# Kernel tuning notes

Measured on AMD Instinct MI355X. Metric: run time of the kernel, lower is better.

Reference implementation:

```python
import jax, jax.numpy as jnp
import numpy as np

B, N, C = 8, 4096, 512

def setup_inputs() -> dict:
    key = jax.random.key(0)
    ks = jax.random.split(key, 6)
    s = 1.0 / np.sqrt(C)
    return {
        "x": jax.random.normal(ks[0], (B, N, C), jnp.float32),
        "Wq": jax.random.normal(ks[1], (C, C), jnp.float32) * s,
        "Wk": jax.random.normal(ks[2], (C, C), jnp.float32) * s,
        "Wv": jax.random.normal(ks[3], (C, C), jnp.float32) * s,
        "W1": jax.random.normal(ks[4], (C, C), jnp.float32) * s,
        "W2": jax.random.normal(ks[5], (C, C), jnp.float32) * s,
    }

def reference(x, Wq, Wk, Wv, W1, W2):
    # torch nn.Linear: y = x @ W.T (bias=False)
    q = x @ Wq.T                      # [B,N,C]
    k = x @ Wk.T
    v = x @ Wv.T
    dim = q.shape[-1]
    q = jax.nn.softmax(q, axis=-1) * (dim ** -0.5)   # softmax over channels
    k = jax.nn.softmax(k, axis=-2)                   # softmax over sequence
    context = jnp.einsum('bnd,bne->bde', k, v)       # [B,C,C]
    attn = jnp.einsum('bnd,bde->bne', q, context)    # [B,N,C]
    x = attn + x
    return (x @ W1.T) @ W2.T + x
```

## Files before the change

kernel.cpp:

```cpp
#include <hip/hip_runtime.h>

typedef unsigned int uint;
typedef __bf16 bf16_t;
typedef bf16_t bf16x8 __attribute__((ext_vector_type(8)));
typedef float floatx4 __attribute__((ext_vector_type(4)));

struct __align__(8) us4 { unsigned short x, y, z, w; };

__device__ __forceinline__ unsigned short f2b(float f) {
    unsigned u = __float_as_uint(f);
    u = u + 0x7FFFu + ((u >> 16) & 1u);
    return (unsigned short)(u >> 16);
}
__device__ __forceinline__ float b2f(unsigned short h) {
    return __uint_as_float(((unsigned)h) << 16);
}

__device__ __forceinline__ void g2l16(const void* g, void* l) {
    __builtin_amdgcn_global_load_lds((__attribute__((address_space(1))) void*)g,
                                     (__attribute__((address_space(3))) void*)l,
                                     16, 0, 0);
}

template <int MODE, int NTN, bool BMS>
__global__ __launch_bounds__(512, 2) void gemm256(
    const unsigned short* __restrict__ A, const unsigned short* __restrict__ B,
    void* __restrict__ O, const unsigned short* __restrict__ R,
    unsigned short* __restrict__ O2, unsigned short* __restrict__ O3,
    float* __restrict__ Sq, float* __restrict__ Sk,
    const float* __restrict__ Sn,
    int K, long long sB, float scale)
{
    __shared__ __attribute__((aligned(16))) unsigned short Ls[4][16384];

    const uint id = blockIdx.x;
    const uint xcd = id & 7;
    const uint g = id >> 3;
    const uint nt = g % NTN;
    const uint mg = g / NTN;
    const uint ms = mg * 8 + xcd;

    int bb, arow0;
    if constexpr (BMS) { bb = (int)(ms & 7); arow0 = bb * 4096 + (int)(ms >> 3) * 256; }
    else               { bb = 0;             arow0 = (int)ms * 256; }
    const int n0 = (int)nt * 256;

    const unsigned short* Bb = B + (long long)bb * sB;
    const int tid = threadIdx.x;
    const int l = tid & 63;
    const int w = tid >> 6;

    const int r0 = tid >> 3;
    const int lc = (tid & 7) ^ (r0 & 7);
    const unsigned short* gsrc = (lc < 4)
        ? A  + (long long)(arow0 + r0) * 512 + lc * 8
        : Bb + (long long)(n0   + r0) * 512 + (lc - 4) * 8;

#define STAGE(bufi, tt) {                                                   \
        const unsigned short* s_ = gsrc + (tt) * 32;                        \
        unsigned short* d_ = &Ls[bufi][0] + tid * 8;                        \
        g2l16(s_,              d_);                                         \
        g2l16(s_ + 64  * 512,  d_ + 4096);                                  \
        g2l16(s_ + 128 * 512,  d_ + 8192);                                  \
        g2l16(s_ + 192 * 512,  d_ + 12288);                                 \
    }

    const int fr = l & 15;
    const int kq = (l >> 4) * 8;
    const int axA = (kq * 2) ^ ((fr & 7) << 4);
    const int axB = axA ^ 64;
    const int wr = w >> 2;
    const int wc = w & 3;

    floatx4 acc[8][4] = {};
    const int NTk = K >> 5;

    STAGE(0, 0); STAGE(1, 1); STAGE(2, 2);
    asm volatile("s_waitcnt vmcnt(8)" ::: "memory");
    __builtin_amdgcn_s_barrier();

    for (int t = 0; t < NTk; ++t) {
        if (t + 3 < NTk) STAGE((t + 3) & 3, t + 3);

        const char* Lb = (const char*)&Ls[t & 3][0];
        const char* pa = Lb + (wr * 128 + fr) * 128 + axA;
        const char* pb = Lb + (wc * 64  + fr) * 128 + axB;

        bf16x8 af[8], bv[4];
#pragma unroll
        for (int i = 0; i < 8; ++i) af[i] = *(const bf16x8*)(pa + i * 2048);
#pragma unroll
        for (int j = 0; j < 4; ++j) bv[j] = *(const bf16x8*)(pb + j * 2048);

        __builtin_amdgcn_s_setprio(1);
#pragma unroll
        for (int i = 0; i < 8; ++i)
#pragma unroll
            for (int j = 0; j < 4; ++j)
                acc[i][j] = __builtin_amdgcn_mfma_f32_16x16x32_bf16(
                    af[i], bv[j], acc[i][j], 0, 0, 0);
        __builtin_amdgcn_s_setprio(0);

        if (t < NTk - 1) {
            if (t + 3 < NTk)      asm volatile("s_waitcnt vmcnt(8)" ::: "memory");
            else if (t + 2 < NTk) asm volatile("s_waitcnt vmcnt(4)" ::: "memory");
            else                  asm volatile("s_waitcnt vmcnt(0)" ::: "memory");
            __builtin_amdgcn_s_barrier();
        }
    }
#undef STAGE

    const int col = l & 15;
    const int rbase = (l >> 4) * 4;
    const int gm0 = arow0 + wr * 128 + rbase;
    const int gn0 = n0 + wc * 64 + col;

    if constexpr (MODE == 4) {
        if (n0 < 512) {
            unsigned short* Oq = (unsigned short*)O;
            float rs[8][4];
#pragma unroll
            for (int i = 0; i < 8; ++i)
#pragma unroll
                for (int r = 0; r < 4; ++r) rs[i][r] = 0.f;
#pragma unroll
            for (int i = 0; i < 8; ++i) {
                int gm = gm0 + i * 16;
#pragma unroll
                for (int j = 0; j < 4; ++j) {
                    int gn = gn0 + j * 16;
#pragma unroll
                    for (int r = 0; r < 4; ++r) {
                        float e = __expf(acc[i][j][r]);
                        rs[i][r] += e;
                        Oq[(long long)(gm + r) * 512 + gn] = f2b(e);
                    }
                }
            }
#pragma unroll
            for (int i = 0; i < 8; ++i)
#pragma unroll
                for (int r = 0; r < 4; ++r) {
                    float v = rs[i][r];
                    v += __shfl_xor(v, 1);
                    v += __shfl_xor(v, 2);
                    v += __shfl_xor(v, 4);
                    v += __shfl_xor(v, 8);
                    if ((l & 15) == 0)
                        atomicAdd(&Sq[gm0 + i * 16 + r], v);
                }
        } else if (n0 < 1024) {
            const int b = arow0 >> 12;
            const int mq0 = (arow0 & 4095) + wr * 128 + rbase;
            float cs[4] = {0.f, 0.f, 0.f, 0.f};
#pragma unroll
            for (int i = 0; i < 8; ++i) {
                int mq = mq0 + i * 16;
#pragma unroll
                for (int j = 0; j < 4; ++j) {
                    int d = gn0 + j * 16 - 512;
                    float e0 = __expf(acc[i][j][0]);
                    float e1 = __expf(acc[i][j][1]);
                    float e2 = __expf(acc[i][j][2]);
                    float e3 = __expf(acc[i][j][3]);
                    cs[j] += e0 + e1 + e2 + e3;
                    us4 pk = { f2b(e0), f2b(e1), f2b(e2), f2b(e3) };
                    *(us4*)(O2 + ((long long)b * 512 + d) * 4096 + mq) = pk;
                }
            }
#pragma unroll
            for (int j = 0; j < 4; ++j) {
                float v = cs[j];
                v += __shfl_xor(v, 16);
                v += __shfl_xor(v, 32);
                if (l < 16)
                    atomicAdd(&Sk[b * 512 + gn0 + j * 16 - 512], v);
            }
        } else {
            const int b = arow0 >> 12;
            const int mq0 = (arow0 & 4095) + wr * 128 + rbase;
#pragma unroll
            for (int i = 0; i < 8; ++i) {
                int mq = mq0 + i * 16;
#pragma unroll
                for (int j = 0; j < 4; ++j) {
                    int e_ = gn0 + j * 16 - 1024;
                    us4 pk = { f2b(acc[i][j][0]), f2b(acc[i][j][1]),
                               f2b(acc[i][j][2]), f2b(acc[i][j][3]) };
                    *(us4*)(O3 + ((long long)b * 512 + e_) * 4096 + mq) = pk;
                }
            }
        }
    } else if constexpr (MODE == 5) {
#pragma unroll
        for (int i = 0; i < 8; ++i) {
            int gm = gm0 + i * 16;
            float invs[4];
#pragma unroll
            for (int r = 0; r < 4; ++r) invs[r] = scale / Sn[gm + r];
#pragma unroll
            for (int j = 0; j < 4; ++j) {
                int gn = gn0 + j * 16;
#pragma unroll
                for (int r = 0; r < 4; ++r) {
                    long long idx = (long long)(gm + r) * 512 + gn;
                    ((unsigned short*)O)[idx] =
                        f2b(acc[i][j][r] * invs[r] + b2f(R[idx]));
                }
            }
        }
    } else {
#pragma unroll
        for (int i = 0; i < 8; ++i) {
            int gm = gm0 + i * 16;
#pragma unroll
            for (int j = 0; j < 4; ++j) {
                int gn = gn0 + j * 16;
#pragma unroll
                for (int r = 0; r < 4; ++r) {
                    long long idx = (long long)(gm + r) * 512 + gn;
                    float v = acc[i][j][r];
                    if constexpr (MODE == 0) {
                        ((unsigned short*)O)[idx] = f2b(v);
                    } else {
                        ((float*)O)[idx] = v + b2f(R[idx]);
                    }
                }
            }
        }
    }
}

__global__ __launch_bounds__(256, 4) void ctx_gemm_sk(
    const unsigned short* __restrict__ V, const unsigned short* __restrict__ Kt,
    float* __restrict__ P)
{
    __shared__ __attribute__((aligned(16))) unsigned short As[128 * 64];
    __shared__ __attribute__((aligned(16))) unsigned short Bs[128 * 64];

    const uint id = blockIdx.x;
    const uint xcd = id & 7;
    const uint g = id >> 3;
    const uint sub = g & 15;
    const int z = (int)(g >> 4) * 8 + (int)xcd;
    const int b = z >> 2;
    const int s = z & 3;
    const int m0 = (int)(sub >> 2) * 128;
    const int n0 = (int)(sub & 3) * 128;

    const unsigned short* Ab = V  + (long long)b * 512 * 4096 + s * 1024;
    const unsigned short* Bb = Kt + (long long)b * 512 * 4096 + s * 1024;

    const int tid = threadIdx.x;
    const int l = tid & 63;
    const int w = tid >> 6;
    const int wm = (w >> 1) * 64;
    const int wn = (w & 1) * 64;

    const int srow = tid >> 3;
    const int scol = (tid & 7) * 8;
    const unsigned short* ga = Ab + (long long)(m0 + srow) * 4096 + scol;
    const unsigned short* gb = Bb + (long long)(n0 + srow) * 4096 + scol;
    unsigned short* la = As + tid * 8;
    unsigned short* lb = Bs + tid * 8;

    const int fr = l & 15;
    const int kq = (l >> 4) * 8;

    floatx4 acc[4][4] = {};

    for (int kt = 0; kt < 1024; kt += 64) {
        __syncthreads();
#pragma unroll
        for (int c = 0; c < 4; ++c) {
            g2l16(ga + (long long)(c * 32) * 4096, la + c * 2048);
            g2l16(gb + (long long)(c * 32) * 4096, lb + c * 2048);
        }
        ga += 64; gb += 64;
        __syncthreads();

#pragma unroll
        for (int h = 0; h < 2; ++h) {
            bf16x8 af[4], bfr[4];
#pragma unroll
            for (int i = 0; i < 4; ++i) {
                af[i]  = *(const bf16x8*)(As + (wm + i * 16 + fr) * 64 + kq + 32 * h);
                bfr[i] = *(const bf16x8*)(Bs + (wn + i * 16 + fr) * 64 + kq + 32 * h);
            }
#pragma unroll
            for (int i = 0; i < 4; ++i)
#pragma unroll
                for (int j = 0; j < 4; ++j)
                    acc[i][j] = __builtin_amdgcn_mfma_f32_16x16x32_bf16(
                        af[i], bfr[j], acc[i][j], 0, 0, 0);
        }
    }

    const int col = l & 15;
    const int rbase = (l >> 4) * 4;
    float* Pb = P + ((long long)z * 16 + (sub >> 2) * 4 + (sub & 3)) * 16384;
#pragma unroll
    for (int i = 0; i < 4; ++i)
#pragma unroll
        for (int j = 0; j < 4; ++j)
#pragma unroll
            for (int r = 0; r < 4; ++r)
                Pb[(wm + i * 16 + rbase + r) * 128 + wn + j * 16 + col] =
                    acc[i][j][r];
}

__global__ __launch_bounds__(256) void ctx_reduce(const float* __restrict__ P,
                                                  const float* __restrict__ Sk,
                                                  unsigned short* __restrict__ Ct)
{
    long long f = (long long)blockIdx.x * 256 + threadIdx.x;
    long long base = f * 4;
    int tile = (int)(base >> 14);
    int lo = (int)(base & 16383);
    int b = tile >> 4;
    int mt = (tile >> 2) & 3;
    int nt = tile & 3;
    float4 s = {0.f, 0.f, 0.f, 0.f};
#pragma unroll
    for (int sp = 0; sp < 4; ++sp) {
        float4 v = *(const float4*)(P + ((long long)(b * 4 + sp) * 16 + mt * 4 + nt) * 16384 + lo);
        s.x += v.x; s.y += v.y; s.z += v.z; s.w += v.w;
    }
    int le = lo >> 7;
    int ld = lo & 127;
    float4 sk = *(const float4*)(Sk + b * 512 + nt * 128 + ld);
    us4 o = { f2b(s.x / sk.x), f2b(s.y / sk.y), f2b(s.z / sk.z), f2b(s.w / sk.w) };
    *(us4*)(Ct + (long long)b * 262144 + (mt * 128 + le) * 512 + nt * 128 + ld) = o;
}

__global__ __launch_bounds__(256) void f32_to_bf16_k(const float* __restrict__ in,
                                                     unsigned short* __restrict__ out)
{
    long long i = ((long long)blockIdx.x * 256 + threadIdx.x) * 4;
    float4 v = *(const float4*)(in + i);
    us4 o = { f2b(v.x), f2b(v.y), f2b(v.z), f2b(v.w) };
    *(us4*)(out + i) = o;
}

struct WPtrs { const float* in[5]; unsigned short* out[5]; };
__global__ __launch_bounds__(256) void conv_weights(WPtrs p)
{
    int which = blockIdx.y;
    long long i = ((long long)blockIdx.x * 256 + threadIdx.x) * 4;
    float4 v = *(const float4*)(p.in[which] + i);
    us4 o = { f2b(v.x), f2b(v.y), f2b(v.z), f2b(v.w) };
    *(us4*)(p.out[which] + i) = o;
}

__global__ __launch_bounds__(256) void zero_f32(float* __restrict__ p)
{
    long long i = ((long long)blockIdx.x * 256 + threadIdx.x) * 4;
    *(float4*)(p + i) = make_float4(0.f, 0.f, 0.f, 0.f);
}

extern "C" void kernel_launch(void* const* d_in, const int* in_sizes, int n_in,
                              void* d_out, int out_size, void* d_ws, size_t ws_size,
                              hipStream_t stream)
{
    (void)in_sizes; (void)n_in; (void)out_size; (void)ws_size;
    const float* x  = (const float*)d_in[0];
    const float* Wq = (const float*)d_in[1];
    const float* Wk = (const float*)d_in[2];
    const float* Wv = (const float*)d_in[3];
    const float* W1 = (const float*)d_in[4];
    const float* W2 = (const float*)d_in[5];
    float* out = (float*)d_out;

    const int Bn = 8, N = 4096, C = 512;
    const long long M  = (long long)Bn * N;
    const long long XE = M * C;

    char* ws = (char*)d_ws;
    size_t off = 0;
    auto carve = [&](size_t bytes) -> void* {
        void* p = ws + off;
        off += (bytes + 255) & ~(size_t)255;
        return p;
    };

    unsigned short* xb   = (unsigned short*)carve(XE * 2);
    unsigned short* wcat = (unsigned short*)carve((size_t)3 * C * C * 2);
    unsigned short* w1b  = (unsigned short*)carve((size_t)C * C * 2);
    unsigned short* w2b  = (unsigned short*)carve((size_t)C * C * 2);
    unsigned short* q    = (unsigned short*)carve(XE * 2);
    unsigned short* kT   = (unsigned short*)carve(XE * 2);
    unsigned short* vT   = (unsigned short*)carve(XE * 2);
    unsigned short* ctxT = (unsigned short*)carve((size_t)Bn * C * C * 2);
    float* Ssum = (float*)carve((size_t)(M + Bn * C) * 4);
    float* Sq = Ssum;
    float* Sk = Ssum + M;
    unsigned short* xr = kT;
    unsigned short* h  = vT;
    float* P = (float*)d_out;

    zero_f32<<<dim3(36), 256, 0, stream>>>(Ssum);

    f32_to_bf16_k<<<dim3((unsigned)(XE / 1024)), dim3(256), 0, stream>>>(x, xb);
    WPtrs wp = { { Wq, Wk, Wv, W1, W2 },
                 { wcat, wcat + C * C, wcat + 2 * C * C, w1b, w2b } };
    conv_weights<<<dim3((C * C) / 1024, 5), dim3(256), 0, stream>>>(wp);

    gemm256<4, 6, false><<<dim3(768), 512, 0, stream>>>(
        xb, wcat, q, nullptr, kT, vT, Sq, Sk, nullptr, C, 0, 0.f);

    ctx_gemm_sk<<<dim3(512), 256, 0, stream>>>(vT, kT, P);
    ctx_reduce<<<dim3(2048), 256, 0, stream>>>(P, Sk, ctxT);

    gemm256<5, 2, true><<<dim3(256), 512, 0, stream>>>(
        q, ctxT, xr, xb, nullptr, nullptr, nullptr, nullptr, Sq,
        C, (long long)C * C, 0.044194173824159216f);

    gemm256<0, 2, false><<<dim3(256), 512, 0, stream>>>(
        xr, w1b, h, nullptr, nullptr, nullptr, nullptr, nullptr, nullptr,
        C, 0, 0.f);

    gemm256<3, 2, false><<<dim3(256), 512, 0, stream>>>(
        h, w2b, out, xr, nullptr, nullptr, nullptr, nullptr, nullptr,
        C, 0, 0.f);
}
```

Baseline: 302.3 us.

## Restructure gemm256 into ping-pong K=64 pipeline and reuse it for context GEMM

```diff
diff --git a/kernel.cpp b/kernel.cpp
--- a/kernel.cpp
+++ b/kernel.cpp
@@ -22,7 +22,7 @@
                                      16, 0, 0);
 }
 
-template <int MODE, int NTN, bool BMS>
+template <int MODE, int NTN, bool BMS, int LD>
 __global__ __launch_bounds__(512, 2) void gemm256(
     const unsigned short* __restrict__ A, const unsigned short* __restrict__ B,
     void* __restrict__ O, const unsigned short* __restrict__ R,
@@ -31,91 +31,161 @@
     const float* __restrict__ Sn,
     int K, long long sB, float scale)
 {
-    __shared__ __attribute__((aligned(16))) unsigned short Ls[4][16384];
+    __shared__ __attribute__((aligned(16))) unsigned short Ls[2][4][8192];
 
     const uint id = blockIdx.x;
-    const uint xcd = id & 7;
-    const uint g = id >> 3;
-    const uint nt = g % NTN;
-    const uint mg = g / NTN;
-    const uint ms = mg * 8 + xcd;
-
-    int bb, arow0;
-    if constexpr (BMS) { bb = (int)(ms & 7); arow0 = bb * 4096 + (int)(ms >> 3) * 256; }
-    else               { bb = 0;             arow0 = (int)ms * 256; }
-    const int n0 = (int)nt * 256;
-
-    const unsigned short* Bb = B + (long long)bb * sB;
     const int tid = threadIdx.x;
     const int l = tid & 63;
     const int w = tid >> 6;
-
-    const int r0 = tid >> 3;
-    const int lc = (tid & 7) ^ (r0 & 7);
-    const unsigned short* gsrc = (lc < 4)
-        ? A  + (long long)(arow0 + r0) * 512 + lc * 8
-        : Bb + (long long)(n0   + r0) * 512 + (lc - 4) * 8;
-
-#define STAGE(bufi, tt) {                                                   \
-        const unsigned short* s_ = gsrc + (tt) * 32;                        \
-        unsigned short* d_ = &Ls[bufi][0] + tid * 8;                        \
-        g2l16(s_,              d_);                                         \
-        g2l16(s_ + 64  * 512,  d_ + 4096);                                  \
-        g2l16(s_ + 128 * 512,  d_ + 8192);                                  \
-        g2l16(s_ + 192 * 512,  d_ + 12288);                                 \
-    }
-
-    const int fr = l & 15;
-    const int kq = (l >> 4) * 8;
-    const int axA = (kq * 2) ^ ((fr & 7) << 4);
-    const int axB = axA ^ 64;
     const int wr = w >> 2;
     const int wc = w & 3;
 
+    int arow0 = 0, n0 = 0, bb = 0;
+    const unsigned short* Ab;
+    const unsigned short* Bbp;
+    long long pbase = 0;
+
+    if constexpr (MODE == 6) {
+        const int mt = (int)(id >> 1) & 1, ntc = (int)id & 1;
+        const int zz = (int)(id >> 2);
+        const int b6 = zz & 7, sk6 = zz >> 3;
+        Ab  = A + ((long long)b6 * 512 + mt  * 256) * 4096 + sk6 * 512;
+        Bbp = B + ((long long)b6 * 512 + ntc * 256) * 4096 + sk6 * 512;
+        pbase = (long long)(b6 * 32 + sk6 * 4 + mt * 2 + ntc) * 65536;
+    } else {
+        const uint xcd = id & 7;
+        const uint g = id >> 3;
+        const uint nt = g % NTN;
+        const uint mg = g / NTN;
+        const uint ms = mg * 8 + xcd;
+        if constexpr (BMS) { bb = (int)(ms & 7); arow0 = bb * 4096 + (int)(ms >> 3) * 256; }
+        else               { bb = 0;             arow0 = (int)ms * 256; }
+        n0 = (int)nt * 256;
+        Ab  = A + (long long)arow0 * LD;
+        Bbp = B + (long long)bb * sB + (long long)n0 * LD;
+    }
+
+    const int n0i = w * 128 + l;
+    const int n1i = n0i + 64;
+    const unsigned short* pA0 = Ab  + (long long)(n0i >> 2) * LD + ((n0i & 3) ^ ((n0i >> 3) & 3)) * 8;
+    const unsigned short* pA1 = Ab  + (long long)(n1i >> 2) * LD + ((n1i & 3) ^ ((n1i >> 3) & 3)) * 8;
+    const unsigned short* pB0 = Bbp + (long long)(n0i >> 2) * LD + ((n0i & 3) ^ ((n0i >> 3) & 3)) * 8;
+    const unsigned short* pB1 = Bbp + (long long)(n1i >> 2) * LD + ((n1i & 3) ^ ((n1i >> 3) & 3)) * 8;
+
+#define STG(bufi, sl, p0, p1, koff) do {                                    \
+        unsigned short* d_ = &Ls[bufi][sl][0] + n0i * 8;                    \
+        g2l16((p0) + (koff), d_);                                           \
+        g2l16((p1) + (koff), d_ + 512);                                     \
+    } while (0)
+
+    const int fr = l & 15;
+    const int c0 = l >> 4;
+    const int swz = (c0 ^ ((fr >> 1) & 3)) << 4;
+    const int aoff = (wr * 128 + fr) * 64 + swz;
+    const int boff = (wc * 64 + fr) * 64 + swz;
+
     floatx4 acc[8][4] = {};
-    const int NTk = K >> 5;
-
-    STAGE(0, 0); STAGE(1, 1); STAGE(2, 2);
+    const int NTk = K >> 6;
+
+    STG(0, 0, pA0, pA1, 0);
+    STG(0, 2, pB0, pB1, 0);
+    STG(0, 1, pA0, pA1, 32);
+    STG(0, 3, pB0, pB1, 32);
+    if (NTk > 1) {
+        STG(1, 0, pA0, pA1, 64);
+        STG(1, 2, pB0, pB1, 64);
+    }
     asm volatile("s_waitcnt vmcnt(8)" ::: "memory");
     __builtin_amdgcn_s_barrier();
 
     for (int t = 0; t < NTk; ++t) {
-        if (t + 3 < NTk) STAGE((t + 3) & 3, t + 3);
-
-        const char* Lb = (const char*)&Ls[t & 3][0];
-        const char* pa = Lb + (wr * 128 + fr) * 128 + axA;
-        const char* pb = Lb + (wc * 64  + fr) * 128 + axB;
-
-        bf16x8 af[8], bv[4];
-#pragma unroll
-        for (int i = 0; i < 8; ++i) af[i] = *(const bf16x8*)(pa + i * 2048);
-#pragma unroll
-        for (int j = 0; j < 4; ++j) bv[j] = *(const bf16x8*)(pb + j * 2048);
-
+        const int bi = t & 1;
+        const char* Lb = (const char*)&Ls[bi][0][0];
+        bf16x8 af[8], bv0, bv1, bv2, bv3;
+
+#pragma unroll
+        for (int i = 0; i < 8; ++i)
+            af[i] = *(const bf16x8*)(Lb + 0 * 16384 + aoff + i * 1024);
+        bv0 = *(const bf16x8*)(Lb + 2 * 16384 + boff);
+        bv1 = *(const bf16x8*)(Lb + 2 * 16384 + boff + 1024);
+        if (t + 1 < NTk) STG((t + 1) & 1, 1, pA0, pA1, (t + 1) * 64 + 32);
+        __builtin_amdgcn_s_barrier();
         __builtin_amdgcn_s_setprio(1);
 #pragma unroll
+        for (int i = 0; i < 8; ++i) {
+            acc[i][0] = __builtin_amdgcn_mfma_f32_16x16x32_bf16(af[i], bv0, acc[i][0], 0, 0, 0);
+            acc[i][1] = __builtin_amdgcn_mfma_f32_16x16x32_bf16(af[i], bv1, acc[i][1], 0, 0, 0);
+        }
+        __builtin_amdgcn_s_setprio(0);
+        __builtin_amdgcn_s_barrier();
+
+        bv2 = *(const bf16x8*)(Lb + 2 * 16384 + boff + 2048);
+        bv3 = *(const bf16x8*)(Lb + 2 * 16384 + boff + 3072);
+        if (t + 1 < NTk) STG((t + 1) & 1, 3, pB0, pB1, (t + 1) * 64 + 32);
+        if (t < NTk - 1) asm volatile("s_waitcnt vmcnt(8)" ::: "memory");
+        else             asm volatile("s_waitcnt vmcnt(0)" ::: "memory");
+        __builtin_amdgcn_s_barrier();
+        __builtin_amdgcn_s_setprio(1);
+#pragma unroll
+        for (int i = 0; i < 8; ++i) {
+            acc[i][2] = __builtin_amdgcn_mfma_f32_16x16x32_bf16(af[i], bv2, acc[i][2], 0, 0, 0);
+            acc[i][3] = __builtin_amdgcn_mfma_f32_16x16x32_bf16(af[i], bv3, acc[i][3], 0, 0, 0);
+        }
+        __builtin_amdgcn_s_setprio(0);
+        __builtin_amdgcn_s_barrier();
+
+#pragma unroll
         for (int i = 0; i < 8; ++i)
-#pragma unroll
-            for (int j = 0; j < 4; ++j)
-                acc[i][j] = __builtin_amdgcn_mfma_f32_16x16x32_bf16(
-                    af[i], bv[j], acc[i][j], 0, 0, 0);
+            af[i] = *(const bf16x8*)(Lb + 1 * 16384 + aoff + i * 1024);
+        bv0 = *(const bf16x8*)(Lb + 3 * 16384 + boff);
+        bv1 = *(const bf16x8*)(Lb + 3 * 16384 + boff + 1024);
+        if (t + 2 < NTk) STG(bi, 0, pA0, pA1, (t + 2) * 64);
+        __builtin_amdgcn_s_barrier();
+        __builtin_amdgcn_s_setprio(1);
+#pragma unroll
+        for (int i = 0; i < 8; ++i) {
+            acc[i][0] = __builtin_amdgcn_mfma_f32_16x16x32_bf16(af[i], bv0, acc[i][0], 0, 0, 0);
+            acc[i][1] = __builtin_amdgcn_mfma_f32_16x16x32_bf16(af[i], bv1, acc[i][1], 0, 0, 0);
+        }
         __builtin_amdgcn_s_setprio(0);
-
-        if (t < NTk - 1) {
-            if (t + 3 < NTk)      asm volatile("s_waitcnt vmcnt(8)" ::: "memory");
-            else if (t + 2 < NTk) asm volatile("s_waitcnt vmcnt(4)" ::: "memory");
-            else                  asm volatile("s_waitcnt vmcnt(0)" ::: "memory");
-            __builtin_amdgcn_s_barrier();
-        }
+        __builtin_amdgcn_s_barrier();
+
+        bv2 = *(const bf16x8*)(Lb + 3 * 16384 + boff + 2048);
+        bv3 = *(const bf16x8*)(Lb + 3 * 16384 + boff + 3072);
+        if (t + 2 < NTk) STG(bi, 2, pB0, pB1, (t + 2) * 64);
+        if (t < NTk - 2)       asm volatile("s_waitcnt vmcnt(8)" ::: "memory");
+        else if (t == NTk - 2) asm volatile("s_waitcnt vmcnt(4)" ::: "memory");
+        __builtin_amdgcn_s_barrier();
+        __builtin_amdgcn_s_setprio(1);
+#pragma unroll
+        for (int i = 0; i < 8; ++i) {
+            acc[i][2] = __builtin_amdgcn_mfma_f32_16x16x32_bf16(af[i], bv2, acc[i][2], 0, 0, 0);
+            acc[i][3] = __builtin_amdgcn_mfma_f32_16x16x32_bf16(af[i], bv3, acc[i][3], 0, 0, 0);
+        }
+        __builtin_amdgcn_s_setprio(0);
+        __builtin_amdgcn_s_barrier();
     }
-#undef STAGE
+#undef STG
 
     const int col = l & 15;
     const int rbase = (l >> 4) * 4;
     const int gm0 = arow0 + wr * 128 + rbase;
     const int gn0 = n0 + wc * 64 + col;
 
-    if constexpr (MODE == 4) {
+    if constexpr (MODE == 6) {
+        float* Pb = (float*)O + pbase;
+#pragma unroll
+        for (int i = 0; i < 8; ++i) {
+            int lr = wr * 128 + i * 16 + rbase;
+#pragma unroll
+            for (int j = 0; j < 4; ++j) {
+                int lc = wc * 64 + j * 16 + col;
+#pragma unroll
+                for (int r = 0; r < 4; ++r)
+                    Pb[(lr + r) * 256 + lc] = acc[i][j][r];
+            }
+        }
+    } else if constexpr (MODE == 4) {
         if (n0 < 512) {
             unsigned short* Oq = (unsigned short*)O;
             float rs[8][4];
@@ -231,106 +301,25 @@
     }
 }
 
-__global__ __launch_bounds__(256, 4) void ctx_gemm_sk(
-    const unsigned short* __restrict__ V, const unsigned short* __restrict__ Kt,
-    float* __restrict__ P)
-{
-    __shared__ __attribute__((aligned(16))) unsigned short As[128 * 64];
-    __shared__ __attribute__((aligned(16))) unsigned short Bs[128 * 64];
-
-    const uint id = blockIdx.x;
-    const uint xcd = id & 7;
-    const uint g = id >> 3;
-    const uint sub = g & 15;
-    const int z = (int)(g >> 4) * 8 + (int)xcd;
-    const int b = z >> 2;
-    const int s = z & 3;
-    const int m0 = (int)(sub >> 2) * 128;
-    const int n0 = (int)(sub & 3) * 128;
-
-    const unsigned short* Ab = V  + (long long)b * 512 * 4096 + s * 1024;
-    const unsigned short* Bb = Kt + (long long)b * 512 * 4096 + s * 1024;
-
-    const int tid = threadIdx.x;
-    const int l = tid & 63;
-    const int w = tid >> 6;
-    const int wm = (w >> 1) * 64;
-    const int wn = (w & 1) * 64;
-
-    const int srow = tid >> 3;
-    const int scol = (tid & 7) * 8;
-    const unsigned short* ga = Ab + (long long)(m0 + srow) * 4096 + scol;
-    const unsigned short* gb = Bb + (long long)(n0 + srow) * 4096 + scol;
-    unsigned short* la = As + tid * 8;
-    unsigned short* lb = Bs + tid * 8;
-
-    const int fr = l & 15;
-    const int kq = (l >> 4) * 8;
-
-    floatx4 acc[4][4] = {};
-
-    for (int kt = 0; kt < 1024; kt += 64) {
-        __syncthreads();
-#pragma unroll
-        for (int c = 0; c < 4; ++c) {
-            g2l16(ga + (long long)(c * 32) * 4096, la + c * 2048);
-            g2l16(gb + (long long)(c * 32) * 4096, lb + c * 2048);
-        }
-        ga += 64; gb += 64;
-        __syncthreads();
-
-#pragma unroll
-        for (int h = 0; h < 2; ++h) {
-            bf16x8 af[4], bfr[4];
-#pragma unroll
-            for (int i = 0; i < 4; ++i) {
-                af[i]  = *(const bf16x8*)(As + (wm + i * 16 + fr) * 64 + kq + 32 * h);
-                bfr[i] = *(const bf16x8*)(Bs + (wn + i * 16 + fr) * 64 + kq + 32 * h);
-            }
-#pragma unroll
-            for (int i = 0; i < 4; ++i)
-#pragma unroll
-                for (int j = 0; j < 4; ++j)
-                    acc[i][j] = __builtin_amdgcn_mfma_f32_16x16x32_bf16(
-                        af[i], bfr[j], acc[i][j], 0, 0, 0);
-        }
-    }
-
-    const int col = l & 15;
-    const int rbase = (l >> 4) * 4;
-    float* Pb = P + ((long long)z * 16 + (sub >> 2) * 4 + (sub & 3)) * 16384;
-#pragma unroll
-    for (int i = 0; i < 4; ++i)
-#pragma unroll
-        for (int j = 0; j < 4; ++j)
-#pragma unroll
-            for (int r = 0; r < 4; ++r)
-                Pb[(wm + i * 16 + rbase + r) * 128 + wn + j * 16 + col] =
-                    acc[i][j][r];
-}
-
 __global__ __launch_bounds__(256) void ctx_reduce(const float* __restrict__ P,
                                                   const float* __restrict__ Sk,
                                                   unsigned short* __restrict__ Ct)
 {
     long long f = (long long)blockIdx.x * 256 + threadIdx.x;
-    long long base = f * 4;
-    int tile = (int)(base >> 14);
-    int lo = (int)(base & 16383);
-    int b = tile >> 4;
-    int mt = (tile >> 2) & 3;
-    int nt = tile & 3;
+    int b = (int)(f >> 16);
+    int e = (int)(f >> 7) & 511;
+    int d = ((int)f & 127) * 4;
+    int mt = e >> 8, nt2 = d >> 8, lr = e & 255, lc = d & 255;
+    long long base0 = (long long)(b * 32 + mt * 2 + nt2) * 65536 + lr * 256 + lc;
     float4 s = {0.f, 0.f, 0.f, 0.f};
 #pragma unroll
-    for (int sp = 0; sp < 4; ++sp) {
-        float4 v = *(const float4*)(P + ((long long)(b * 4 + sp) * 16 + mt * 4 + nt) * 16384 + lo);
+    for (int sp = 0; sp < 8; ++sp) {
+        float4 v = *(const float4*)(P + base0 + (long long)sp * 4 * 65536);
         s.x += v.x; s.y += v.y; s.z += v.z; s.w += v.w;
     }
-    int le = lo >> 7;
-    int ld = lo & 127;
-    float4 sk = *(const float4*)(Sk + b * 512 + nt * 128 + ld);
+    float4 sk = *(const float4*)(Sk + b * 512 + d);
     us4 o = { f2b(s.x / sk.x), f2b(s.y / sk.y), f2b(s.z / sk.z), f2b(s.w / sk.w) };
-    *(us4*)(Ct + (long long)b * 262144 + (mt * 128 + le) * 512 + nt * 128 + ld) = o;
+    *(us4*)(Ct + ((long long)b * 512 + e) * 512 + d) = o;
 }
 
 __global__ __launch_bounds__(256) void f32_to_bf16_k(const float* __restrict__ in,
@@ -405,21 +394,23 @@
                  { wcat, wcat + C * C, wcat + 2 * C * C, w1b, w2b } };
     conv_weights<<<dim3((C * C) / 1024, 5), dim3(256), 0, stream>>>(wp);
 
-    gemm256<4, 6, false><<<dim3(768), 512, 0, stream>>>(
-        xb, wcat, q, nullptr, kT, vT, Sq, Sk, nullptr, C, 0, 0.f);
-
-    ctx_gemm_sk<<<dim3(512), 256, 0, stream>>>(vT, kT, P);
+    gemm256<4, 6, false, 512><<<dim3(768), 512, 0, stream>>>(
+        xb, wcat, q, nullptr, kT, vT, Sq, Sk, nullptr, 512, 0, 0.f);
+
+    gemm256<6, 1, false, 4096><<<dim3(256), 512, 0, stream>>>(
+        vT, kT, P, nullptr, nullptr, nullptr, nullptr, nullptr, nullptr,
+        512, 0, 0.f);
     ctx_reduce<<<dim3(2048), 256, 0, stream>>>(P, Sk, ctxT);
 
-    gemm256<5, 2, true><<<dim3(256), 512, 0, stream>>>(
+    gemm256<5, 2, true, 512><<<dim3(256), 512, 0, stream>>>(
         q, ctxT, xr, xb, nullptr, nullptr, nullptr, nullptr, Sq,
-        C, (long long)C * C, 0.044194173824159216f);
-
-    gemm256<0, 2, false><<<dim3(256), 512, 0, stream>>>(
+        512, (long long)C * C, 0.044194173824159216f);
+
+    gemm256<0, 2, false, 512><<<dim3(256), 512, 0, stream>>>(
         xr, w1b, h, nullptr, nullptr, nullptr, nullptr, nullptr, nullptr,
-        C, 0, 0.f);
-
-    gemm256<3, 2, false><<<dim3(256), 512, 0, stream>>>(
+        512, 0, 0.f);
+
+    gemm256<3, 2, false, 512><<<dim3(256), 512, 0, stream>>>(
         h, w2b, out, xr, nullptr, nullptr, nullptr, nullptr, nullptr,
-        C, 0, 0.f);
-}
+        512, 0, 0.f);
+}
```

Result: slower. 320.1 us (+5.9%).
